# Optimization experiments

Hardware: AMD Instinct MI355X
Metric: run time of the kernel (lower is better)

Reference implementation:

```python
import jax, jax.numpy as jnp
import numpy as np

B, T, D = 8, 2048, 1024
DK, DV = 1024, 1024


def setup_inputs() -> dict:
    key = jax.random.key(0)
    ks = jax.random.split(key, 11)
    s = 0.02
    return {
        "query": jax.random.normal(ks[0], (B, T, D), jnp.float32),
        "keys": jax.random.normal(ks[1], (B, T, D), jnp.float32),
        "values": jax.random.normal(ks[2], (B, T, D), jnp.float32),
        "Wq": jax.random.normal(ks[3], (D, DK), jnp.float32) * s,
        "bq": jnp.zeros((DK,), jnp.float32),
        "Wk": jax.random.normal(ks[4], (D, DK), jnp.float32) * s,
        "bk": jnp.zeros((DK,), jnp.float32),
        "Wv": jax.random.normal(ks[5], (D, DV), jnp.float32) * s,
        "bv": jnp.zeros((DV,), jnp.float32),
        "Wo": jax.random.normal(ks[6], (DV, D), jnp.float32) * s,
        "bo": jnp.zeros((D,), jnp.float32),
        "apply_mask": 1,
    }


def reference(query, keys, values, Wq, bq, Wk, bk, Wv, bv, Wo, bo, apply_mask):
    # input projections
    q = query @ Wq + bq   # [B, T, DK]
    k = keys @ Wk + bk    # [B, T, DK]
    v = values @ Wv + bv  # [B, T, DV]
    dk = jnp.asarray(DK, jnp.float32)
    # explicit full score matrix, as in the original (non-flash) module
    scores = jnp.einsum("btd,bsd->bts", q, k) / jnp.sqrt(dk)  # [B, T, T]
    if apply_mask:
        Tq = q.shape[1]
        causal = jnp.triu(jnp.ones((Tq, Tq), bool), 1)  # True above diagonal
        scores = jnp.where(causal[None, :, :], -jnp.inf, scores)
    weights = jax.nn.softmax(scores, axis=-1)
    context = jnp.einsum("bts,bsd->btd", weights, v)  # [B, T, DV]
    return context @ Wo + bo  # [B, T, D]
```

## Files before the change

### kernel.cpp

```cpp
#include <hip/hip_runtime.h>
#include <hip/hip_bf16.h>


typedef __attribute__((ext_vector_type(8))) short bf16x8;
typedef __attribute__((ext_vector_type(4))) float f32x4;

#define DEVI __device__ __forceinline__
#define VM_GATE(n) asm volatile("s_waitcnt vmcnt(" #n ")" ::: "memory")

DEVI unsigned short f2bf(float f) {
  union { float f; unsigned u; } v; v.f = f;
  unsigned r = v.u + 0x7FFFu + ((v.u >> 16) & 1u);
  return (unsigned short)(r >> 16);
}

DEVI void load_lds16(const void* g, void* l) {
  __builtin_amdgcn_global_load_lds(
      (const __attribute__((address_space(1))) unsigned int*)g,
      (__attribute__((address_space(3))) unsigned int*)l,
      16, 0, 0);
}

constexpr int BM = 256, BN = 256, BK = 64;

DEVI void stage_chunk(char* chunk, const unsigned short* src, long ldx,
                      int kbase, int tid) {
#pragma unroll
  for (int i = 0; i < 2; ++i) {
    int tloc = i * 512 + tid;
    int r = tloc >> 2, ps = tloc & 3;
    int q = (ps - (r >> 1)) & 3;
    load_lds16(src + (size_t)r * ldx + kbase + q * 8,
               chunk + (i * 512 + (tid & 0x1C0)) * 16);
  }
}

DEVI bf16x8 frag(const char* chunk, int r, int q0) {
  int sp = (q0 + (r >> 1)) & 3;
  return *(const bf16x8*)(chunk + r * 64 + sp * 16);
}

template<bool OUT_F32, bool OUT_TRANS, bool DO_BIAS, bool DO_SCALE,
         bool DO_CSKIP, bool DO_KCLAMP>
__global__ __launch_bounds__(512, 2) void gemm_k(
    const unsigned short* __restrict__ Ab, long lda, long sAz,
    const unsigned short* __restrict__ Bt, long ldb, long sBz,
    void* __restrict__ Cp, long ldc, long sCz,
    const float* __restrict__ bias, float scale,
    const int* __restrict__ maskp, int Kdim)
{
  const int nx = gridDim.x, ny = gridDim.y;
  int bid = (blockIdx.z * ny + blockIdx.y) * nx + blockIdx.x;
  const int nwg = nx * ny * (int)gridDim.z;
  if ((nwg & 7) == 0) bid = (bid & 7) * (nwg >> 3) + (bid >> 3);
  const int bx = bid % nx;
  const int t1 = bid / nx;
  const int by = t1 % ny;
  const int z  = t1 / ny;

  const int n0 = bx * BN;
  const int m0 = by * BM;
  if constexpr (DO_CSKIP) {
    if (maskp[0] && n0 > m0 + (BM - 1)) return;
  }
  int Keff = Kdim;
  if constexpr (DO_KCLAMP) {
    if (maskp[0]) Keff = min(Kdim, m0 + BM);
  }

  __shared__ alignas(16) char LDSb[2][2][2][16384];

  const int tid  = threadIdx.x;
  const int lane = tid & 63;
  const int w    = tid >> 6;
  const int wr   = w >> 2, wc = w & 3;
  const int la   = lane & 15;
  const int q0   = lane >> 4;

  f32x4 acc[8][4];
  const f32x4 z4 = {0.f, 0.f, 0.f, 0.f};
#pragma unroll
  for (int mi = 0; mi < 8; ++mi)
#pragma unroll
    for (int ni = 0; ni < 4; ++ni) acc[mi][ni] = z4;

  const unsigned short* Ag0 = Ab + (size_t)z * sAz + (size_t)m0 * lda;
  const unsigned short* Bg0 = Bt + (size_t)z * sBz + (size_t)n0 * ldb;

  stage_chunk(LDSb[0][0][0], Ag0, lda, 0,  tid);
  stage_chunk(LDSb[0][1][0], Bg0, ldb, 0,  tid);
  stage_chunk(LDSb[0][0][1], Ag0, lda, 32, tid);
  stage_chunk(LDSb[0][1][1], Bg0, ldb, 32, tid);

  const int nt = Keff / BK;
  for (int t = 0; t < nt; ++t) {
    const int buf = t & 1, nb = buf ^ 1;
    const bool pf = (t + 1 < nt);
    const int kb = (t + 1) * BK;
    const char* Ak0 = LDSb[buf][0][0];
    const char* Bk0 = LDSb[buf][1][0];
    const char* Ak1 = LDSb[buf][0][1];
    const char* Bk1 = LDSb[buf][1][1];
    bf16x8 bfv0[4], bfv1[4], af[4];

    VM_GATE(4);
    __builtin_amdgcn_s_barrier();
    __builtin_amdgcn_sched_barrier(0);
#pragma unroll
    for (int ni = 0; ni < 4; ++ni) bfv0[ni] = frag(Bk0, wc * 64 + ni * 16 + la, q0);
#pragma unroll
    for (int mi = 0; mi < 4; ++mi) af[mi] = frag(Ak0, wr * 128 + mi * 16 + la, q0);
    if (pf) stage_chunk((char*)LDSb[nb][0][0], Ag0, lda, kb, tid);
    __builtin_amdgcn_s_setprio(1);
#pragma unroll
    for (int mi = 0; mi < 4; ++mi)
#pragma unroll
      for (int ni = 0; ni < 4; ++ni)
        acc[mi][ni] = __builtin_amdgcn_mfma_f32_16x16x32_bf16(af[mi], bfv0[ni], acc[mi][ni], 0, 0, 0);
    __builtin_amdgcn_s_setprio(0);

    __builtin_amdgcn_s_barrier();
    __builtin_amdgcn_sched_barrier(0);
#pragma unroll
    for (int mi = 0; mi < 4; ++mi) af[mi] = frag(Ak0, wr * 128 + 64 + mi * 16 + la, q0);
    if (pf) stage_chunk((char*)LDSb[nb][1][0], Bg0, ldb, kb, tid);
    __builtin_amdgcn_s_setprio(1);
#pragma unroll
    for (int mi = 0; mi < 4; ++mi)
#pragma unroll
      for (int ni = 0; ni < 4; ++ni)
        acc[4 + mi][ni] = __builtin_amdgcn_mfma_f32_16x16x32_bf16(af[mi], bfv0[ni], acc[4 + mi][ni], 0, 0, 0);
    __builtin_amdgcn_s_setprio(0);

    if (pf) { VM_GATE(4); } else { VM_GATE(0); }
    __builtin_amdgcn_s_barrier();
    __builtin_amdgcn_sched_barrier(0);
#pragma unroll
    for (int ni = 0; ni < 4; ++ni) bfv1[ni] = frag(Bk1, wc * 64 + ni * 16 + la, q0);
#pragma unroll
    for (int mi = 0; mi < 4; ++mi) af[mi] = frag(Ak1, wr * 128 + mi * 16 + la, q0);
    if (pf) stage_chunk((char*)LDSb[nb][0][1], Ag0, lda, kb + 32, tid);
    __builtin_amdgcn_s_setprio(1);
#pragma unroll
    for (int mi = 0; mi < 4; ++mi)
#pragma unroll
      for (int ni = 0; ni < 4; ++ni)
        acc[mi][ni] = __builtin_amdgcn_mfma_f32_16x16x32_bf16(af[mi], bfv1[ni], acc[mi][ni], 0, 0, 0);
    __builtin_amdgcn_s_setprio(0);

    __builtin_amdgcn_s_barrier();
    __builtin_amdgcn_sched_barrier(0);
#pragma unroll
    for (int mi = 0; mi < 4; ++mi) af[mi] = frag(Ak1, wr * 128 + 64 + mi * 16 + la, q0);
    if (pf) stage_chunk((char*)LDSb[nb][1][1], Bg0, ldb, kb + 32, tid);
    __builtin_amdgcn_s_setprio(1);
#pragma unroll
    for (int mi = 0; mi < 4; ++mi)
#pragma unroll
      for (int ni = 0; ni < 4; ++ni)
        acc[4 + mi][ni] = __builtin_amdgcn_mfma_f32_16x16x32_bf16(af[mi], bfv1[ni], acc[4 + mi][ni], 0, 0, 0);
    __builtin_amdgcn_s_setprio(0);
  }

#pragma unroll
  for (int ni = 0; ni < 4; ++ni) {
    const int n = n0 + wc * 64 + ni * 16 + la;
    float bv = 0.f;
    if constexpr (DO_BIAS) bv = bias[n];
#pragma unroll
    for (int mi = 0; mi < 8; ++mi) {
      const int m = m0 + wr * 128 + mi * 16 + (q0 << 2);
      f32x4 c = acc[mi][ni];
      if constexpr (DO_SCALE) c = c * scale;
      if constexpr (DO_BIAS)  c = c + bv;
      if constexpr (OUT_TRANS) {
        unsigned short* C = (unsigned short*)Cp + (size_t)z * sCz + (size_t)n * ldc + m;
        ushort4 h;
        h.x = f2bf(c[0]); h.y = f2bf(c[1]); h.z = f2bf(c[2]); h.w = f2bf(c[3]);
        *(ushort4*)C = h;
      } else if constexpr (OUT_F32) {
        float* C = (float*)Cp + (size_t)z * sCz + (size_t)m * ldc + n;
#pragma unroll
        for (int j = 0; j < 4; ++j) C[(size_t)j * ldc] = c[j];
      } else {
        unsigned short* C = (unsigned short*)Cp + (size_t)z * sCz + (size_t)m * ldc + n;
#pragma unroll
        for (int j = 0; j < 4; ++j) C[(size_t)j * ldc] = f2bf(c[j]);
      }
    }
  }
}

__global__ __launch_bounds__(256) void cvt_k(
    const float* __restrict__ q, const float* __restrict__ k,
    const float* __restrict__ v, unsigned short* __restrict__ xq,
    unsigned short* __restrict__ xk, unsigned short* __restrict__ xv)
{
  const float* s = blockIdx.y == 0 ? q : blockIdx.y == 1 ? k : v;
  unsigned short* d = blockIdx.y == 0 ? xq : blockIdx.y == 1 ? xk : xv;
  const long n4 = 8l * 2048 * 1024 / 4;
  for (long i = (long)blockIdx.x * 256 + threadIdx.x; i < n4;
       i += (long)gridDim.x * 256) {
    float4 a = *(const float4*)(s + i * 4);
    ushort4 h;
    h.x = f2bf(a.x); h.y = f2bf(a.y); h.z = f2bf(a.z); h.w = f2bf(a.w);
    *(ushort4*)(d + i * 4) = h;
  }
}

__global__ __launch_bounds__(256) void wtrans_k(const float* __restrict__ W,
                                                unsigned short* __restrict__ Wt)
{
  __shared__ unsigned short L[64][80];
  const int n0 = blockIdx.x * 64, k0 = blockIdx.y * 64;
  const int tid = threadIdx.x;
#pragma unroll
  for (int p = 0; p < 4; ++p) {
    int idx = tid + p * 256;
    int r = idx >> 4, c4 = idx & 15;
    float4 v = *(const float4*)(W + (size_t)(k0 + r) * 1024 + n0 + c4 * 4);
    L[c4 * 4 + 0][r] = f2bf(v.x);
    L[c4 * 4 + 1][r] = f2bf(v.y);
    L[c4 * 4 + 2][r] = f2bf(v.z);
    L[c4 * 4 + 3][r] = f2bf(v.w);
  }
  __syncthreads();
#pragma unroll
  for (int p = 0; p < 2; ++p) {
    int idx = tid + p * 256;
    int n = idx >> 3, c8 = idx & 7;
    int4 v = *(const int4*)(&L[n][c8 * 8]);
    *(int4*)(Wt + (size_t)(n0 + n) * 1024 + k0 + c8 * 8) = v;
  }
}

__global__ __launch_bounds__(256) void softmax_k(float* __restrict__ S,
                                                 const int* __restrict__ maskp)
{
  const int row = blockIdx.x;
  const int t = row & 2047;
  const int msk = maskp[0];
  const int lim  = msk ? (t + 1) : 2048;
  const int wlim = msk ? ((t & ~255) + 256) : 2048;
  float* Srow = S + (size_t)row * 2048;
  const int tid = threadIdx.x;
  const int cbase = tid * 8;

  float v[8];
  if (cbase < lim) {
    float4 a = *(const float4*)(Srow + cbase);
    float4 b = *(const float4*)(Srow + cbase + 4);
    v[0] = a.x; v[1] = a.y; v[2] = a.z; v[3] = a.w;
    v[4] = b.x; v[5] = b.y; v[6] = b.z; v[7] = b.w;
#pragma unroll
    for (int j = 0; j < 8; ++j)
      if (cbase + j >= lim) v[j] = -__builtin_inff();
  } else {
#pragma unroll
    for (int j = 0; j < 8; ++j) v[j] = -__builtin_inff();
  }

  float mx = v[0];
#pragma unroll
  for (int j = 1; j < 8; ++j) mx = fmaxf(mx, v[j]);
#pragma unroll
  for (int off = 32; off; off >>= 1) mx = fmaxf(mx, __shfl_xor(mx, off, 64));

  __shared__ float redm[4], reds[4];
  const int wid = tid >> 6;
  if ((tid & 63) == 0) redm[wid] = mx;
  __syncthreads();
  mx = fmaxf(fmaxf(redm[0], redm[1]), fmaxf(redm[2], redm[3]));

  float e[8], s = 0.f;
#pragma unroll
  for (int j = 0; j < 8; ++j) { e[j] = __expf(v[j] - mx); s += e[j]; }
#pragma unroll
  for (int off = 32; off; off >>= 1) s += __shfl_xor(s, off, 64);
  if ((tid & 63) == 0) reds[wid] = s;
  __syncthreads();
  s = reds[0] + reds[1] + reds[2] + reds[3];
  const float inv = 1.0f / s;

  if (cbase < wlim) {
    unsigned short* Prow = (unsigned short*)Srow;
    unsigned pk[4];
#pragma unroll
    for (int q = 0; q < 4; ++q)
      pk[q] = (unsigned)f2bf(e[2 * q] * inv) | ((unsigned)f2bf(e[2 * q + 1] * inv) << 16);
    int4 o; o.x = (int)pk[0]; o.y = (int)pk[1]; o.z = (int)pk[2]; o.w = (int)pk[3];
    *(int4*)(Prow + (size_t)cbase) = o;
  }
}

extern "C" void kernel_launch(void* const* d_in, const int* in_sizes, int n_in,
                              void* d_out, int out_size, void* d_ws, size_t ws_size,
                              hipStream_t stream)
{
  const float* query  = (const float*)d_in[0];
  const float* keys   = (const float*)d_in[1];
  const float* values = (const float*)d_in[2];
  const float* Wq = (const float*)d_in[3];
  const float* bq = (const float*)d_in[4];
  const float* Wk = (const float*)d_in[5];
  const float* bk = (const float*)d_in[6];
  const float* Wv = (const float*)d_in[7];
  const float* bv = (const float*)d_in[8];
  const float* Wo = (const float*)d_in[9];
  const float* bo = (const float*)d_in[10];
  const int* maskp = (const int*)d_in[11];
  float* out = (float*)d_out;

  char* ws = (char*)d_ws;
  const size_t MB = 1ull << 20;
  unsigned short* wt_q = (unsigned short*)(ws + 0 * MB);
  unsigned short* wt_k = (unsigned short*)(ws + 2 * MB);
  unsigned short* wt_v = (unsigned short*)(ws + 4 * MB);
  unsigned short* wt_o = (unsigned short*)(ws + 6 * MB);
  unsigned short* Qb   = (unsigned short*)(ws + 8 * MB);
  unsigned short* Kb   = (unsigned short*)(ws + 40 * MB);
  unsigned short* Vt   = (unsigned short*)(ws + 72 * MB);
  float*          S    = (float*)(ws + 104 * MB);
  unsigned short* Xq   = (unsigned short*)(ws + 104 * MB);
  unsigned short* Xk   = (unsigned short*)(ws + 136 * MB);
  unsigned short* Xv   = (unsigned short*)(ws + 168 * MB);
  unsigned short* ctx  = Qb;

  const dim3 blk(512);
  const long sXT = 2048l * 1024;

  wtrans_k<<<dim3(16, 16), dim3(256), 0, stream>>>(Wq, wt_q);
  wtrans_k<<<dim3(16, 16), dim3(256), 0, stream>>>(Wk, wt_k);
  wtrans_k<<<dim3(16, 16), dim3(256), 0, stream>>>(Wv, wt_v);
  wtrans_k<<<dim3(16, 16), dim3(256), 0, stream>>>(Wo, wt_o);
  cvt_k<<<dim3(4096, 3), dim3(256), 0, stream>>>(query, keys, values, Xq, Xk, Xv);

  gemm_k<false, false, true, false, false, false><<<dim3(4, 8, 8), blk, 0, stream>>>(
      Xq, 1024, sXT, wt_q, 1024, 0, Qb, 1024, sXT, bq, 1.f, nullptr, 1024);
  gemm_k<false, false, true, false, false, false><<<dim3(4, 8, 8), blk, 0, stream>>>(
      Xk, 1024, sXT, wt_k, 1024, 0, Kb, 1024, sXT, bk, 1.f, nullptr, 1024);
  gemm_k<false, true, true, false, false, false><<<dim3(4, 8, 8), blk, 0, stream>>>(
      Xv, 1024, sXT, wt_v, 1024, 0, Vt, 2048, 1024l * 2048, bv, 1.f, nullptr, 1024);

  gemm_k<true, false, false, true, true, false><<<dim3(8, 8, 8), blk, 0, stream>>>(
      Qb, 1024, sXT, Kb, 1024, sXT, S, 2048, 2048l * 2048, nullptr, 0.03125f, maskp, 1024);

  softmax_k<<<dim3(16384), dim3(256), 0, stream>>>(S, maskp);

  gemm_k<false, false, false, false, false, true><<<dim3(4, 8, 8), blk, 0, stream>>>(
      (unsigned short*)S, 4096, 2048l * 4096, Vt, 2048, 1024l * 2048,
      ctx, 1024, sXT, nullptr, 1.f, maskp, 2048);

  gemm_k<true, false, true, false, false, false><<<dim3(4, 8, 8), blk, 0, stream>>>(
      ctx, 1024, sXT, wt_o, 1024, 0, out, 1024, sXT, bo, 1.f, nullptr, 1024);
}
```

Measured before the change: 374.3 us.

## Fuse fp32-to-bf16 input conversion into projection GEMM A-operand loading

Removes the separate conversion kernel that turned query/keys/values into bf16 buffers. The projection GEMMs now load fp32 A tiles into registers, convert them with packed bf16 conversion instructions, and write them swizzled into LDS, overlapping this with the MFMA work. This saves one full read/write pass over three 64MB inputs. In exchange the GEMM reads twice the A bytes, uses more registers, and adds an lgkmcnt wait per iteration.

```diff
diff --git a/kernel.cpp b/kernel.cpp
--- a/kernel.cpp
+++ b/kernel.cpp
@@ -7,11 +7,18 @@
 
 #define DEVI __device__ __forceinline__
 #define VM_GATE(n) asm volatile("s_waitcnt vmcnt(" #n ")" ::: "memory")
+#define LGKM0()    asm volatile("s_waitcnt lgkmcnt(0)" ::: "memory")
 
 DEVI unsigned short f2bf(float f) {
   union { float f; unsigned u; } v; v.f = f;
   unsigned r = v.u + 0x7FFFu + ((v.u >> 16) & 1u);
   return (unsigned short)(r >> 16);
+}
+
+DEVI unsigned pkbf(float a, float b) {
+  unsigned r;
+  asm("v_cvt_pk_bf16_f32 %0, %1, %2" : "=v"(r) : "v"(a), "v"(b));
+  return r;
 }
 
 DEVI void load_lds16(const void* g, void* l) {
@@ -40,10 +47,36 @@
   return *(const bf16x8*)(chunk + r * 64 + sp * 16);
 }
 
-template<bool OUT_F32, bool OUT_TRANS, bool DO_BIAS, bool DO_SCALE,
+DEVI void a32_load(float4* fr, const float* src, long lda, int kbase, int tid) {
+#pragma unroll
+  for (int j = 0; j < 4; ++j) {
+    int cell = j * 512 + tid;
+    int r = cell >> 3, q = cell & 7;
+    const float* p = src + (size_t)r * lda + kbase + q * 8;
+    fr[2 * j]     = *(const float4*)p;
+    fr[2 * j + 1] = *(const float4*)(p + 4);
+  }
+}
+DEVI void a32_write(char* chunk0, char* chunk1, const float4* fr, int tid) {
+#pragma unroll
+  for (int j = 0; j < 4; ++j) {
+    int cell = j * 512 + tid;
+    int r = cell >> 3, q = cell & 7;
+    int kh = q >> 2, qq = q & 3;
+    int sp = (qq + (r >> 1)) & 3;
+    uint4 u;
+    u.x = pkbf(fr[2 * j].x,     fr[2 * j].y);
+    u.y = pkbf(fr[2 * j].z,     fr[2 * j].w);
+    u.z = pkbf(fr[2 * j + 1].x, fr[2 * j + 1].y);
+    u.w = pkbf(fr[2 * j + 1].z, fr[2 * j + 1].w);
+    *(uint4*)((kh ? chunk1 : chunk0) + r * 64 + sp * 16) = u;
+  }
+}
+
+template<bool A_F32, bool OUT_F32, bool OUT_TRANS, bool DO_BIAS, bool DO_SCALE,
          bool DO_CSKIP, bool DO_KCLAMP>
 __global__ __launch_bounds__(512, 2) void gemm_k(
-    const unsigned short* __restrict__ Ab, long lda, long sAz,
+    const void* __restrict__ Ap, long lda, long sAz,
     const unsigned short* __restrict__ Bt, long ldb, long sBz,
     void* __restrict__ Cp, long ldc, long sCz,
     const float* __restrict__ bias, float scale,
@@ -84,13 +117,25 @@
 #pragma unroll
     for (int ni = 0; ni < 4; ++ni) acc[mi][ni] = z4;
 
-  const unsigned short* Ag0 = Ab + (size_t)z * sAz + (size_t)m0 * lda;
+  const unsigned short* Ag0 = (const unsigned short*)Ap + (size_t)z * sAz + (size_t)m0 * lda;
+  const float*          Af0 = (const float*)Ap + (size_t)z * sAz + (size_t)m0 * lda;
   const unsigned short* Bg0 = Bt + (size_t)z * sBz + (size_t)n0 * ldb;
 
-  stage_chunk(LDSb[0][0][0], Ag0, lda, 0,  tid);
-  stage_chunk(LDSb[0][1][0], Bg0, ldb, 0,  tid);
-  stage_chunk(LDSb[0][0][1], Ag0, lda, 32, tid);
-  stage_chunk(LDSb[0][1][1], Bg0, ldb, 32, tid);
+  float4 fr[8];
+
+  if constexpr (A_F32) {
+    a32_load(fr, Af0, lda, 0, tid);
+    stage_chunk((char*)LDSb[0][1][0], Bg0, ldb, 0,  tid);
+    stage_chunk((char*)LDSb[0][1][1], Bg0, ldb, 32, tid);
+    VM_GATE(4);
+    a32_write((char*)LDSb[0][0][0], (char*)LDSb[0][0][1], fr, tid);
+    LGKM0();
+  } else {
+    stage_chunk((char*)LDSb[0][0][0], Ag0, lda, 0,  tid);
+    stage_chunk((char*)LDSb[0][1][0], Bg0, ldb, 0,  tid);
+    stage_chunk((char*)LDSb[0][0][1], Ag0, lda, 32, tid);
+    stage_chunk((char*)LDSb[0][1][1], Bg0, ldb, 32, tid);
+  }
 
   const int nt = Keff / BK;
   for (int t = 0; t < nt; ++t) {
@@ -103,14 +148,17 @@
     const char* Bk1 = LDSb[buf][1][1];
     bf16x8 bfv0[4], bfv1[4], af[4];
 
-    VM_GATE(4);
+    if constexpr (A_F32) { VM_GATE(2); } else { VM_GATE(4); }
     __builtin_amdgcn_s_barrier();
     __builtin_amdgcn_sched_barrier(0);
 #pragma unroll
     for (int ni = 0; ni < 4; ++ni) bfv0[ni] = frag(Bk0, wc * 64 + ni * 16 + la, q0);
 #pragma unroll
     for (int mi = 0; mi < 4; ++mi) af[mi] = frag(Ak0, wr * 128 + mi * 16 + la, q0);
-    if (pf) stage_chunk((char*)LDSb[nb][0][0], Ag0, lda, kb, tid);
+    if (pf) {
+      if constexpr (A_F32) a32_load(fr, Af0, lda, kb, tid);
+      else stage_chunk((char*)LDSb[nb][0][0], Ag0, lda, kb, tid);
+    }
     __builtin_amdgcn_s_setprio(1);
 #pragma unroll
     for (int mi = 0; mi < 4; ++mi)
@@ -132,14 +180,23 @@
         acc[4 + mi][ni] = __builtin_amdgcn_mfma_f32_16x16x32_bf16(af[mi], bfv0[ni], acc[4 + mi][ni], 0, 0, 0);
     __builtin_amdgcn_s_setprio(0);
 
-    if (pf) { VM_GATE(4); } else { VM_GATE(0); }
+    if constexpr (A_F32) {
+      if (pf) { VM_GATE(2); } else { VM_GATE(0); }
+    } else {
+      if (pf) { VM_GATE(4); } else { VM_GATE(0); }
+    }
     __builtin_amdgcn_s_barrier();
     __builtin_amdgcn_sched_barrier(0);
 #pragma unroll
     for (int ni = 0; ni < 4; ++ni) bfv1[ni] = frag(Bk1, wc * 64 + ni * 16 + la, q0);
 #pragma unroll
     for (int mi = 0; mi < 4; ++mi) af[mi] = frag(Ak1, wr * 128 + mi * 16 + la, q0);
-    if (pf) stage_chunk((char*)LDSb[nb][0][1], Ag0, lda, kb + 32, tid);
+    if (pf) {
+      if constexpr (A_F32)
+        a32_write((char*)LDSb[nb][0][0], (char*)LDSb[nb][0][1], fr, tid);
+      else
+        stage_chunk((char*)LDSb[nb][0][1], Ag0, lda, kb + 32, tid);
+    }
     __builtin_amdgcn_s_setprio(1);
 #pragma unroll
     for (int mi = 0; mi < 4; ++mi)
@@ -160,6 +217,9 @@
       for (int ni = 0; ni < 4; ++ni)
         acc[4 + mi][ni] = __builtin_amdgcn_mfma_f32_16x16x32_bf16(af[mi], bfv1[ni], acc[4 + mi][ni], 0, 0, 0);
     __builtin_amdgcn_s_setprio(0);
+    if constexpr (A_F32) {
+      if (pf) { LGKM0(); __builtin_amdgcn_sched_barrier(0); }
+    }
   }
 
 #pragma unroll
@@ -188,23 +248,6 @@
         for (int j = 0; j < 4; ++j) C[(size_t)j * ldc] = f2bf(c[j]);
       }
     }
-  }
-}
-
-__global__ __launch_bounds__(256) void cvt_k(
-    const float* __restrict__ q, const float* __restrict__ k,
-    const float* __restrict__ v, unsigned short* __restrict__ xq,
-    unsigned short* __restrict__ xk, unsigned short* __restrict__ xv)
-{
-  const float* s = blockIdx.y == 0 ? q : blockIdx.y == 1 ? k : v;
-  unsigned short* d = blockIdx.y == 0 ? xq : blockIdx.y == 1 ? xk : xv;
-  const long n4 = 8l * 2048 * 1024 / 4;
-  for (long i = (long)blockIdx.x * 256 + threadIdx.x; i < n4;
-       i += (long)gridDim.x * 256) {
-    float4 a = *(const float4*)(s + i * 4);
-    ushort4 h;
-    h.x = f2bf(a.x); h.y = f2bf(a.y); h.z = f2bf(a.z); h.w = f2bf(a.w);
-    *(ushort4*)(d + i * 4) = h;
   }
 }
 
@@ -321,9 +364,6 @@
   unsigned short* Kb   = (unsigned short*)(ws + 40 * MB);
   unsigned short* Vt   = (unsigned short*)(ws + 72 * MB);
   float*          S    = (float*)(ws + 104 * MB);
-  unsigned short* Xq   = (unsigned short*)(ws + 104 * MB);
-  unsigned short* Xk   = (unsigned short*)(ws + 136 * MB);
-  unsigned short* Xv   = (unsigned short*)(ws + 168 * MB);
   unsigned short* ctx  = Qb;
 
   const dim3 blk(512);
@@ -333,24 +373,23 @@
   wtrans_k<<<dim3(16, 16), dim3(256), 0, stream>>>(Wk, wt_k);
   wtrans_k<<<dim3(16, 16), dim3(256), 0, stream>>>(Wv, wt_v);
   wtrans_k<<<dim3(16, 16), dim3(256), 0, stream>>>(Wo, wt_o);
-  cvt_k<<<dim3(4096, 3), dim3(256), 0, stream>>>(query, keys, values, Xq, Xk, Xv);
-
-  gemm_k<false, false, true, false, false, false><<<dim3(4, 8, 8), blk, 0, stream>>>(
-      Xq, 1024, sXT, wt_q, 1024, 0, Qb, 1024, sXT, bq, 1.f, nullptr, 1024);
-  gemm_k<false, false, true, false, false, false><<<dim3(4, 8, 8), blk, 0, stream>>>(
-      Xk, 1024, sXT, wt_k, 1024, 0, Kb, 1024, sXT, bk, 1.f, nullptr, 1024);
-  gemm_k<false, true, true, false, false, false><<<dim3(4, 8, 8), blk, 0, stream>>>(
-      Xv, 1024, sXT, wt_v, 1024, 0, Vt, 2048, 1024l * 2048, bv, 1.f, nullptr, 1024);
-
-  gemm_k<true, false, false, true, true, false><<<dim3(8, 8, 8), blk, 0, stream>>>(
+
+  gemm_k<true, false, false, true, false, false, false><<<dim3(4, 8, 8), blk, 0, stream>>>(
+      query, 1024, sXT, wt_q, 1024, 0, Qb, 1024, sXT, bq, 1.f, nullptr, 1024);
+  gemm_k<true, false, false, true, false, false, false><<<dim3(4, 8, 8), blk, 0, stream>>>(
+      keys, 1024, sXT, wt_k, 1024, 0, Kb, 1024, sXT, bk, 1.f, nullptr, 1024);
+  gemm_k<true, false, true, true, false, false, false><<<dim3(4, 8, 8), blk, 0, stream>>>(
+      values, 1024, sXT, wt_v, 1024, 0, Vt, 2048, 1024l * 2048, bv, 1.f, nullptr, 1024);
+
+  gemm_k<false, true, false, false, true, true, false><<<dim3(8, 8, 8), blk, 0, stream>>>(
       Qb, 1024, sXT, Kb, 1024, sXT, S, 2048, 2048l * 2048, nullptr, 0.03125f, maskp, 1024);
 
   softmax_k<<<dim3(16384), dim3(256), 0, stream>>>(S, maskp);
 
-  gemm_k<false, false, false, false, false, true><<<dim3(4, 8, 8), blk, 0, stream>>>(
+  gemm_k<false, false, false, false, false, false, true><<<dim3(4, 8, 8), blk, 0, stream>>>(
       (unsigned short*)S, 4096, 2048l * 4096, Vt, 2048, 1024l * 2048,
       ctx, 1024, sXT, nullptr, 1.f, maskp, 2048);
 
-  gemm_k<true, false, true, false, false, false><<<dim3(4, 8, 8), blk, 0, stream>>>(
+  gemm_k<false, true, false, true, false, false, false><<<dim3(4, 8, 8), blk, 0, stream>>>(
       ctx, 1024, sXT, wt_o, 1024, 0, out, 1024, sXT, bo, 1.f, nullptr, 1024);
 }
```

After: 354.4 us. 1.06x faster.
